# Performance work log

Measured on AMD Instinct MI355X. Metric: run time of the kernel, lower is better.

## Reference

```python
import jax, jax.numpy as jnp
import numpy as np

K, D, BETA = 64, 512, 100.0
EPS = 1e-12  # F.normalize default eps


def setup_inputs() -> dict:
    key = jax.random.key(0)
    kx, kc = jax.random.split(key)
    x = jax.random.normal(kx, (32, D, 32, 32), dtype=jnp.float32)
    centroids = jax.random.uniform(kc, (K, D), dtype=jnp.float32)  # torch.rand init
    conv_w = 2.0 * BETA * centroids                                # conv weight [K, D] (1x1 kernel)
    conv_b = -BETA * jnp.linalg.norm(centroids, axis=1)            # conv bias [K]
    return {"x": x, "centroids": centroids, "conv_w": conv_w, "conv_b": conv_b}


def reference(x, centroids, conv_w, conv_b):
    N, C = x.shape[:2]
    xf = x.reshape(N, C, -1)                                  # [N, D, P], P = H*W
    # 1x1 conv == per-pixel linear: logits [N, K, P]
    logits = jnp.einsum('ndp,kd->nkp', xf, conv_w) + conv_b[None, :, None]
    a = jax.nn.softmax(logits, axis=1)                        # soft assignment over clusters
    # residual-sum collapses algebraically:
    # vlad[n,k,d] = sum_p a[n,k,p]*x[n,d,p] - (sum_p a[n,k,p]) * c[k,d]
    vlad = jnp.einsum('nkp,ndp->nkd', a, xf) - a.sum(-1)[:, :, None] * centroids[None]
    # intra-normalize per cluster (dim=2), then flatten and L2-normalize
    vlad = vlad / jnp.maximum(jnp.linalg.norm(vlad, axis=2, keepdims=True), EPS)
    vlad = vlad.reshape(N, -1)
    vlad = vlad / jnp.maximum(jnp.linalg.norm(vlad, axis=1, keepdims=True), EPS)
    return vlad
```

## Files before the change

kernel.cpp:

```cpp
#include <hip/hip_runtime.h>
#include <math.h>


namespace {

constexpr int NI   = 32;
constexpr int DIMC = 512;
constexpr int KCL  = 64;
constexpr int PIXN = 1024;
constexpr float EPSF = 1e-12f;

#define AS1 __attribute__((address_space(1)))
#define AS3 __attribute__((address_space(3)))

__device__ __forceinline__ void glds16(const float* g, float* l) {
  __builtin_amdgcn_global_load_lds((const AS1 void*)g, (AS3 void*)l, 16, 0, 0);
}

__global__ __launch_bounds__(256) void k0_wt(const float* __restrict__ w,
                                             float* __restrict__ wt) {
  const int i = blockIdx.x * 256 + threadIdx.x;
  wt[i] = w[(size_t)(i & 63) * DIMC + (i >> 6)];
}

__global__ __launch_bounds__(256, 2) void k1a_logits(
    const float* __restrict__ x, const float* __restrict__ wt,
    const float* __restrict__ conv_b, float* __restrict__ A)
{
  __shared__ float smem[16384];
  float* const xs0 = smem;
  float* const wl0 = smem + 8192;
  float* const scr = smem;

  const int tid = threadIdx.x;
  const int w  = __builtin_amdgcn_readfirstlane(tid >> 6);
  const int l  = tid & 63;
  const int lk = l & 7, ld = l >> 3;
  const int bid = blockIdx.x;
  const int xcd = bid & 7, rest = bid >> 3;
  const int n  = xcd + ((rest & 3) << 3);
  const int pg = rest >> 2;
  const int pb = pg << 6;

  const float* xn = x + (size_t)n * DIMC * PIXN + pb;

#pragma unroll
  for (int s = 0; s < 4; ++s) {
    const int i = s * 256 + tid;
    glds16(xn + (size_t)(i >> 4) * PIXN + ((i & 15) << 2), xs0 + (i << 2));
    glds16(wt + (i << 2), wl0 + (i << 2));
  }

  float acc[8][8];
#pragma unroll
  for (int i = 0; i < 8; ++i)
#pragma unroll
    for (int j = 0; j < 8; ++j) acc[i][j] = 0.0f;

  for (int ch = 0; ch < 8; ++ch) {
    const int cur = ch & 1;
    __syncthreads();
    if (ch < 7) {
      const float* xc = xn + (size_t)((ch + 1) * 64) * PIXN;
      const float* wc = wt + (ch + 1) * 4096;
#pragma unroll
      for (int s = 0; s < 4; ++s) {
        const int i = s * 256 + tid;
        glds16(xc + (size_t)(i >> 4) * PIXN + ((i & 15) << 2),
               xs0 + (cur ^ 1) * 4096 + (i << 2));
        glds16(wc + (i << 2), wl0 + (cur ^ 1) * 4096 + (i << 2));
      }
    }
    const float* wr = wl0 + cur * 4096 + (w << 10) + (lk << 3);
    const float* xr = xs0 + cur * 4096 + (w << 10) + (ld << 3);
#pragma unroll 4
    for (int dd = 0; dd < 16; ++dd) {
      const float4 wa = *reinterpret_cast<const float4*>(wr + (dd << 6));
      const float4 wb = *reinterpret_cast<const float4*>(wr + (dd << 6) + 4);
      const float4 xa = *reinterpret_cast<const float4*>(xr + (dd << 6));
      const float4 xb = *reinterpret_cast<const float4*>(xr + (dd << 6) + 4);
      const float wv[8] = {wa.x, wa.y, wa.z, wa.w, wb.x, wb.y, wb.z, wb.w};
      const float xv[8] = {xa.x, xa.y, xa.z, xa.w, xb.x, xb.y, xb.z, xb.w};
#pragma unroll
      for (int i = 0; i < 8; ++i)
#pragma unroll
        for (int j = 0; j < 8; ++j)
          acc[i][j] = fmaf(wv[i], xv[j], acc[i][j]);
    }
  }
  __syncthreads();

#define TST(RB)                                                              \
  do {                                                                       \
    _Pragma("unroll") for (int i = 0; i < 8; ++i) {                          \
      *reinterpret_cast<float4*>((RB) + ((2 * i) << 8) + (l << 2)) =         \
          make_float4(acc[i][0], acc[i][1], acc[i][2], acc[i][3]);           \
      *reinterpret_cast<float4*>((RB) + ((2 * i + 1) << 8) + (l << 2)) =     \
          make_float4(acc[i][4], acc[i][5], acc[i][6], acc[i][7]);           \
    }                                                                        \
  } while (0)
#define TADD(RB)                                                             \
  do {                                                                       \
    _Pragma("unroll") for (int i = 0; i < 8; ++i) {                          \
      const float4 t0 = *reinterpret_cast<const float4*>(                    \
          (RB) + ((2 * i) << 8) + (l << 2));                                 \
      const float4 t1 = *reinterpret_cast<const float4*>(                    \
          (RB) + ((2 * i + 1) << 8) + (l << 2));                             \
      acc[i][0] += t0.x; acc[i][1] += t0.y; acc[i][2] += t0.z;               \
      acc[i][3] += t0.w; acc[i][4] += t1.x; acc[i][5] += t1.y;               \
      acc[i][6] += t1.z; acc[i][7] += t1.w;                                  \
    }                                                                        \
  } while (0)

  if (w == 1) TST(scr);
  if (w == 3) TST(scr + 4096);
  __syncthreads();
  if (w == 0) TADD(scr);
  if (w == 2) TADD(scr + 4096);
  __syncthreads();
  if (w == 2) TST(scr);
  __syncthreads();

  if (w == 0) {
    TADD(scr);
    const float4 b0 = *reinterpret_cast<const float4*>(conv_b + (lk << 3));
    const float4 b1 = *reinterpret_cast<const float4*>(conv_b + (lk << 3) + 4);
    const float bv[8] = {b0.x, b0.y, b0.z, b0.w, b1.x, b1.y, b1.z, b1.w};
#pragma unroll
    for (int i = 0; i < 8; ++i)
#pragma unroll
      for (int j = 0; j < 8; ++j) acc[i][j] += bv[i];
    float m[8], S[8];
#pragma unroll
    for (int j = 0; j < 8; ++j) {
      m[j] = acc[0][j];
#pragma unroll
      for (int i = 1; i < 8; ++i) m[j] = fmaxf(m[j], acc[i][j]);
      m[j] = fmaxf(m[j], __shfl_xor(m[j], 1, 64));
      m[j] = fmaxf(m[j], __shfl_xor(m[j], 2, 64));
      m[j] = fmaxf(m[j], __shfl_xor(m[j], 4, 64));
      S[j] = 0.0f;
#pragma unroll
      for (int i = 0; i < 8; ++i) {
        acc[i][j] = __expf(acc[i][j] - m[j]);
        S[j] += acc[i][j];
      }
      S[j] += __shfl_xor(S[j], 1, 64);
      S[j] += __shfl_xor(S[j], 2, 64);
      S[j] += __shfl_xor(S[j], 4, 64);
      S[j] = 1.0f / S[j];
    }
#pragma unroll
    for (int j = 0; j < 8; ++j) {
      float* op = A + ((size_t)n * PIXN + pb + (ld << 3) + j) * KCL + (lk << 3);
      *reinterpret_cast<float4*>(op) =
          make_float4(acc[0][j] * S[j], acc[1][j] * S[j],
                      acc[2][j] * S[j], acc[3][j] * S[j]);
      *reinterpret_cast<float4*>(op + 4) =
          make_float4(acc[4][j] * S[j], acc[5][j] * S[j],
                      acc[6][j] * S[j], acc[7][j] * S[j]);
    }
  }
#undef TST
#undef TADD
}

__global__ __launch_bounds__(512, 2) void k2a_vlad(
    const float* __restrict__ x, const float* __restrict__ A,
    const float* __restrict__ cent, float* __restrict__ out,
    float* __restrict__ ssqp)
{
  __shared__ float smem[18432];
  float* const aL0 = smem;
  float* const xL0 = smem + 8192;
  float* const scr = smem;

  const int tid = threadIdx.x;
  const int w  = __builtin_amdgcn_readfirstlane(tid >> 6);
  const int l  = tid & 63;
  const int lk = l & 7, ld = l >> 3;
  const int bid = blockIdx.x;
  const int xcd = bid & 7, rest = bid >> 3;
  const int n  = xcd + ((rest & 3) << 3);
  const int dt = rest >> 2;
  const int d0 = dt << 6;

  const float* an = A + (size_t)n * PIXN * KCL;
  const int dl = tid & 63, pq = tid >> 6;
  const float* xg = x + ((size_t)n * DIMC + d0 + dl) * PIXN + (pq << 3);

  glds16(an + (tid << 2), aL0 + (tid << 2));
  glds16(an + ((tid + 512) << 2), aL0 + ((tid + 512) << 2));
  float4 rx0 = *reinterpret_cast<const float4*>(xg);
  float4 rx1 = *reinterpret_cast<const float4*>(xg + 4);
  {
    float* xw = xL0 + (pq << 9) + dl;
    xw[0]   = rx0.x; xw[64]  = rx0.y; xw[128] = rx0.z; xw[192] = rx0.w;
    xw[256] = rx1.x; xw[320] = rx1.y; xw[384] = rx1.z; xw[448] = rx1.w;
  }
  __syncthreads();

  float acc[8][8], sacc[8];
#pragma unroll
  for (int i = 0; i < 8; ++i) {
    sacc[i] = 0.0f;
#pragma unroll
    for (int j = 0; j < 8; ++j) acc[i][j] = 0.0f;
  }

  for (int ch = 0; ch < 16; ++ch) {
    const int cur = ch & 1;
    const float* aLc = aL0 + cur * 4096;
    const float* xLc = xL0 + cur * 4096;
    if (ch < 15) {
      const float* an2 = an + (size_t)(ch + 1) * 4096;
      glds16(an2 + (tid << 2), aL0 + (cur ^ 1) * 4096 + (tid << 2));
      glds16(an2 + ((tid + 512) << 2),
             aL0 + (cur ^ 1) * 4096 + ((tid + 512) << 2));
      rx0 = *reinterpret_cast<const float4*>(xg + (ch + 1) * 64);
      rx1 = *reinterpret_cast<const float4*>(xg + (ch + 1) * 64 + 4);
    }
#pragma unroll
    for (int st = 0; st < 8; ++st) {
      const int p = (w << 3) + st;
      const float4 a0 = *reinterpret_cast<const float4*>(aLc + (p << 6) + (lk << 3));
      const float4 a1 = *reinterpret_cast<const float4*>(aLc + (p << 6) + (lk << 3) + 4);
      const float4 x0 = *reinterpret_cast<const float4*>(xLc + (p << 6) + (ld << 3));
      const float4 x1 = *reinterpret_cast<const float4*>(xLc + (p << 6) + (ld << 3) + 4);
      const float av[8] = {a0.x, a0.y, a0.z, a0.w, a1.x, a1.y, a1.z, a1.w};
      const float xv[8] = {x0.x, x0.y, x0.z, x0.w, x1.x, x1.y, x1.z, x1.w};
#pragma unroll
      for (int i = 0; i < 8; ++i) {
        sacc[i] += av[i];
#pragma unroll
        for (int j = 0; j < 8; ++j)
          acc[i][j] = fmaf(av[i], xv[j], acc[i][j]);
      }
    }
    if (ch < 15) {
      float* xw = xL0 + (cur ^ 1) * 4096 + (pq << 9) + dl;
      xw[0]   = rx0.x; xw[64]  = rx0.y; xw[128] = rx0.z; xw[192] = rx0.w;
      xw[256] = rx1.x; xw[320] = rx1.y; xw[384] = rx1.z; xw[448] = rx1.w;
    }
    __syncthreads();
  }

#define TST(RB)                                                              \
  do {                                                                       \
    _Pragma("unroll") for (int i = 0; i < 8; ++i) {                          \
      *reinterpret_cast<float4*>((RB) + ((2 * i) << 8) + (l << 2)) =         \
          make_float4(acc[i][0], acc[i][1], acc[i][2], acc[i][3]);           \
      *reinterpret_cast<float4*>((RB) + ((2 * i + 1) << 8) + (l << 2)) =     \
          make_float4(acc[i][4], acc[i][5], acc[i][6], acc[i][7]);           \
    }                                                                        \
    *reinterpret_cast<float4*>((RB) + (16 << 8) + (l << 2)) =                \
        make_float4(sacc[0], sacc[1], sacc[2], sacc[3]);                     \
    *reinterpret_cast<float4*>((RB) + (17 << 8) + (l << 2)) =                \
        make_float4(sacc[4], sacc[5], sacc[6], sacc[7]);                     \
  } while (0)
#define TADD(RB)                                                             \
  do {                                                                       \
    _Pragma("unroll") for (int i = 0; i < 8; ++i) {                          \
      const float4 t0 = *reinterpret_cast<const float4*>(                    \
          (RB) + ((2 * i) << 8) + (l << 2));                                 \
      const float4 t1 = *reinterpret_cast<const float4*>(                    \
          (RB) + ((2 * i + 1) << 8) + (l << 2));                             \
      acc[i][0] += t0.x; acc[i][1] += t0.y; acc[i][2] += t0.z;               \
      acc[i][3] += t0.w; acc[i][4] += t1.x; acc[i][5] += t1.y;               \
      acc[i][6] += t1.z; acc[i][7] += t1.w;                                  \
    }                                                                        \
    const float4 s0 = *reinterpret_cast<const float4*>(                      \
        (RB) + (16 << 8) + (l << 2));                                        \
    const float4 s1 = *reinterpret_cast<const float4*>(                      \
        (RB) + (17 << 8) + (l << 2));                                        \
    sacc[0] += s0.x; sacc[1] += s0.y; sacc[2] += s0.z; sacc[3] += s0.w;      \
    sacc[4] += s1.x; sacc[5] += s1.y; sacc[6] += s1.z; sacc[7] += s1.w;      \
  } while (0)

  if (w >= 4) TST(scr + (w - 4) * 4608);
  __syncthreads();
  if (w < 4) TADD(scr + w * 4608);
  __syncthreads();
  if (w == 2) TST(scr);
  if (w == 3) TST(scr + 4608);
  __syncthreads();
  if (w < 2) TADD(scr + w * 4608);
  __syncthreads();
  if (w == 1) TST(scr);
  __syncthreads();

  if (w == 0) {
    TADD(scr);
#pragma unroll
    for (int i = 0; i < 8; ++i) {
      const int k = (lk << 3) + i;
      const float s = sacc[i];
      const float* cp = cent + (size_t)k * DIMC + d0 + (ld << 3);
      const float4 c0 = *reinterpret_cast<const float4*>(cp);
      const float4 c1 = *reinterpret_cast<const float4*>(cp + 4);
      float r[8];
      r[0] = acc[i][0] - s * c0.x; r[1] = acc[i][1] - s * c0.y;
      r[2] = acc[i][2] - s * c0.z; r[3] = acc[i][3] - s * c0.w;
      r[4] = acc[i][4] - s * c1.x; r[5] = acc[i][5] - s * c1.y;
      r[6] = acc[i][6] - s * c1.z; r[7] = acc[i][7] - s * c1.w;
      float* op = out + ((size_t)n * KCL + k) * DIMC + d0 + (ld << 3);
      *reinterpret_cast<float4*>(op)     = make_float4(r[0], r[1], r[2], r[3]);
      *reinterpret_cast<float4*>(op + 4) = make_float4(r[4], r[5], r[6], r[7]);
      float q = 0.0f;
#pragma unroll
      for (int j = 0; j < 8; ++j) q = fmaf(r[j], r[j], q);
      q += __shfl_xor(q, 8, 64);
      q += __shfl_xor(q, 16, 64);
      q += __shfl_xor(q, 32, 64);
      if (ld == 0) ssqp[((size_t)n * KCL + k) * 8 + dt] = q;
    }
  }
#undef TST
#undef TADD
}

__global__ __launch_bounds__(256) void k2c_norm(
    const float* __restrict__ ssqp, float* __restrict__ out)
{
  __shared__ float invs[64];
  __shared__ float gsh;
  const int tid = threadIdx.x;
  const int n  = blockIdx.x >> 3;
  const int kc = blockIdx.x & 7;
  if (tid < 64) {
    float ssq = 0.0f;
#pragma unroll
    for (int dt = 0; dt < 8; ++dt)
      ssq += ssqp[((size_t)n * KCL + tid) * 8 + dt];
    const float inv = 1.0f / fmaxf(sqrtf(ssq), EPSF);
    invs[tid] = inv;
    float rqv = ssq * inv * inv;
#pragma unroll
    for (int off = 32; off > 0; off >>= 1) rqv += __shfl_xor(rqv, off, 64);
    if (tid == 0) gsh = 1.0f / fmaxf(sqrtf(rqv), EPSF);
  }
  __syncthreads();
  const float sc = invs[(kc << 3) + (tid >> 5)] * gsh;
  float* o = out + ((size_t)n * KCL + (kc << 3)) * DIMC + tid * 16;
#pragma unroll
  for (int q = 0; q < 4; ++q) {
    float4 v = *reinterpret_cast<float4*>(o + (q << 2));
    v.x *= sc; v.y *= sc; v.z *= sc; v.w *= sc;
    *reinterpret_cast<float4*>(o + (q << 2)) = v;
  }
}

}

extern "C" void kernel_launch(void* const* d_in, const int* in_sizes, int n_in,
                              void* d_out, int out_size, void* d_ws, size_t ws_size,
                              hipStream_t stream) {
  (void)in_sizes; (void)n_in; (void)out_size; (void)ws_size;
  const float* x      = (const float*)d_in[0];
  const float* cent   = (const float*)d_in[1];
  const float* conv_w = (const float*)d_in[2];
  const float* conv_b = (const float*)d_in[3];
  float* out = (float*)d_out;
  float* ws  = (float*)d_ws;

  float* A    = ws;
  float* wt   = A + (size_t)NI * PIXN * KCL;
  float* ssqp = wt + 32768;

  k0_wt     <<<128, 256, 0, stream>>>(conv_w, wt);
  k1a_logits<<<512, 256, 0, stream>>>(x, wt, conv_b, A);
  k2a_vlad  <<<256, 512, 0, stream>>>(x, A, cent, out, ssqp);
  k2c_norm  <<<256, 256, 0, stream>>>(ssqp, out);
}
```

Measured before the change: 88.81 us.

## Store soft assignments K-major and stream x via direct-to-LDS swizzled loads

The softmax kernel now writes the assignment matrix as [N,K,P] instead of [N,P,K], with an XOR-swizzled column order. This lets the VLAD kernel load both A and x tiles in pixel-contiguous rows through global_load_lds, with no register staging or transposed LDS stores for x. The inner product loop now reads float4 along pixels with swizzled offsets to avoid LDS bank conflicts. The cost is a less coalesced store pattern in the softmax kernel and more complex indexing.

```diff
diff --git a/kernel.cpp b/kernel.cpp
--- a/kernel.cpp
+++ b/kernel.cpp
@@ -150,15 +150,21 @@
       S[j] += __shfl_xor(S[j], 4, 64);
       S[j] = 1.0f / S[j];
     }
-#pragma unroll
-    for (int j = 0; j < 8; ++j) {
-      float* op = A + ((size_t)n * PIXN + pb + (ld << 3) + j) * KCL + (lk << 3);
-      *reinterpret_cast<float4*>(op) =
-          make_float4(acc[0][j] * S[j], acc[1][j] * S[j],
-                      acc[2][j] * S[j], acc[3][j] * S[j]);
-      *reinterpret_cast<float4*>(op + 4) =
-          make_float4(acc[4][j] * S[j], acc[5][j] * S[j],
-                      acc[6][j] * S[j], acc[7][j] * S[j]);
+    const int bq = ((ld << 1) ^ lk) & ~1;
+#pragma unroll
+    for (int i = 0; i < 8; ++i) {
+      const float4 lo = make_float4(acc[i][0] * S[0], acc[i][1] * S[1],
+                                    acc[i][2] * S[2], acc[i][3] * S[3]);
+      const float4 hi = make_float4(acc[i][4] * S[4], acc[i][5] * S[5],
+                                    acc[i][6] * S[6], acc[i][7] * S[7]);
+      float* arow = A + ((size_t)n * KCL + (lk << 3) + i) * PIXN + pb + (bq << 2);
+      if (lk & 1) {
+        *reinterpret_cast<float4*>(arow)     = hi;
+        *reinterpret_cast<float4*>(arow + 4) = lo;
+      } else {
+        *reinterpret_cast<float4*>(arow)     = lo;
+        *reinterpret_cast<float4*>(arow + 4) = hi;
+      }
     }
   }
 #undef TST
@@ -185,20 +191,16 @@
   const int dt = rest >> 2;
   const int d0 = dt << 6;
 
-  const float* an = A + (size_t)n * PIXN * KCL;
-  const int dl = tid & 63, pq = tid >> 6;
-  const float* xg = x + ((size_t)n * DIMC + d0 + dl) * PIXN + (pq << 3);
-
-  glds16(an + (tid << 2), aL0 + (tid << 2));
-  glds16(an + ((tid + 512) << 2), aL0 + ((tid + 512) << 2));
-  float4 rx0 = *reinterpret_cast<const float4*>(xg);
-  float4 rx1 = *reinterpret_cast<const float4*>(xg + 4);
-  {
-    float* xw = xL0 + (pq << 9) + dl;
-    xw[0]   = rx0.x; xw[64]  = rx0.y; xw[128] = rx0.z; xw[192] = rx0.w;
-    xw[256] = rx1.x; xw[320] = rx1.y; xw[384] = rx1.z; xw[448] = rx1.w;
-  }
-  __syncthreads();
+  const float* an = A + (size_t)n * (KCL * PIXN);
+  const float* xn = x + ((size_t)n * DIMC + d0) * PIXN;
+  const int i0 = tid, i1 = tid + 512;
+  const int xq0 = ((i0 & 15) ^ (i0 >> 7)) << 2;
+  const int xq1 = (((i1 & 15) ^ (i1 >> 7)) & 15) << 2;
+
+  glds16(an + (size_t)(i0 >> 4) * PIXN + ((i0 & 15) << 2), aL0 + (i0 << 2));
+  glds16(an + (size_t)(i1 >> 4) * PIXN + ((i1 & 15) << 2), aL0 + (i1 << 2));
+  glds16(xn + (size_t)(i0 >> 4) * PIXN + xq0, xL0 + (i0 << 2));
+  glds16(xn + (size_t)(i1 >> 4) * PIXN + xq1, xL0 + (i1 << 2));
 
   float acc[8][8], sacc[8];
 #pragma unroll
@@ -207,40 +209,44 @@
 #pragma unroll
     for (int j = 0; j < 8; ++j) acc[i][j] = 0.0f;
   }
+  __syncthreads();
 
   for (int ch = 0; ch < 16; ++ch) {
     const int cur = ch & 1;
     const float* aLc = aL0 + cur * 4096;
     const float* xLc = xL0 + cur * 4096;
     if (ch < 15) {
-      const float* an2 = an + (size_t)(ch + 1) * 4096;
-      glds16(an2 + (tid << 2), aL0 + (cur ^ 1) * 4096 + (tid << 2));
-      glds16(an2 + ((tid + 512) << 2),
-             aL0 + (cur ^ 1) * 4096 + ((tid + 512) << 2));
-      rx0 = *reinterpret_cast<const float4*>(xg + (ch + 1) * 64);
-      rx1 = *reinterpret_cast<const float4*>(xg + (ch + 1) * 64 + 4);
-    }
-#pragma unroll
-    for (int st = 0; st < 8; ++st) {
-      const int p = (w << 3) + st;
-      const float4 a0 = *reinterpret_cast<const float4*>(aLc + (p << 6) + (lk << 3));
-      const float4 a1 = *reinterpret_cast<const float4*>(aLc + (p << 6) + (lk << 3) + 4);
-      const float4 x0 = *reinterpret_cast<const float4*>(xLc + (p << 6) + (ld << 3));
-      const float4 x1 = *reinterpret_cast<const float4*>(xLc + (p << 6) + (ld << 3) + 4);
-      const float av[8] = {a0.x, a0.y, a0.z, a0.w, a1.x, a1.y, a1.z, a1.w};
-      const float xv[8] = {x0.x, x0.y, x0.z, x0.w, x1.x, x1.y, x1.z, x1.w};
+      const int c2 = (ch + 1) * 64;
+      float* aLn = aL0 + (cur ^ 1) * 4096;
+      float* xLn = xL0 + (cur ^ 1) * 4096;
+      glds16(an + (size_t)(i0 >> 4) * PIXN + c2 + ((i0 & 15) << 2), aLn + (i0 << 2));
+      glds16(an + (size_t)(i1 >> 4) * PIXN + c2 + ((i1 & 15) << 2), aLn + (i1 << 2));
+      glds16(xn + (size_t)(i0 >> 4) * PIXN + c2 + xq0, xLn + (i0 << 2));
+      glds16(xn + (size_t)(i1 >> 4) * PIXN + c2 + xq1, xLn + (i1 << 2));
+    }
+#pragma unroll
+    for (int q = 0; q < 2; ++q) {
+      const int pq = (w << 1) + q;
+      float4 af[8], xf[8];
+#pragma unroll
+      for (int i = 0; i < 8; ++i)
+        af[i] = *reinterpret_cast<const float4*>(
+            aLc + (((lk << 3) + i) << 6) + ((pq ^ lk) << 2));
+#pragma unroll
+      for (int jd = 0; jd < 8; ++jd)
+        xf[jd] = *reinterpret_cast<const float4*>(
+            xLc + (((ld << 3) + jd) << 6) + ((pq ^ ld) << 2));
 #pragma unroll
       for (int i = 0; i < 8; ++i) {
-        sacc[i] += av[i];
-#pragma unroll
-        for (int j = 0; j < 8; ++j)
-          acc[i][j] = fmaf(av[i], xv[j], acc[i][j]);
+        sacc[i] += ((af[i].x + af[i].y) + af[i].z) + af[i].w;
+#pragma unroll
+        for (int jd = 0; jd < 8; ++jd) {
+          acc[i][jd] = fmaf(af[i].x, xf[jd].x, acc[i][jd]);
+          acc[i][jd] = fmaf(af[i].y, xf[jd].y, acc[i][jd]);
+          acc[i][jd] = fmaf(af[i].z, xf[jd].z, acc[i][jd]);
+          acc[i][jd] = fmaf(af[i].w, xf[jd].w, acc[i][jd]);
+        }
       }
-    }
-    if (ch < 15) {
-      float* xw = xL0 + (cur ^ 1) * 4096 + (pq << 9) + dl;
-      xw[0]   = rx0.x; xw[64]  = rx0.y; xw[128] = rx0.z; xw[192] = rx0.w;
-      xw[256] = rx1.x; xw[320] = rx1.y; xw[384] = rx1.z; xw[448] = rx1.w;
     }
     __syncthreads();
   }
```

New measurement: 92.31 us. 3.9% more time.
